# Kernel optimization log

Hardware: AMD Instinct MI355X
Metric: run time of the kernel (lower is better)

The kernel has to match this reference:

```python
import jax, jax.numpy as jnp
import numpy as np

B, T, N, E, F_IN = 2, 8, 4000, 40000, 32
H, C, HL, FH = 4, 64, 128, 128  # heads, gat_hidden, lstm_hidden, fusion_hidden


def setup_inputs() -> dict:
    key = jax.random.key(0)
    ks = jax.random.split(key, 14)
    def nrm(i, shape, s=0.05):
        return jax.random.normal(ks[i], shape, jnp.float32) * s
    return {
        "x_seq": jax.random.normal(ks[0], (B, T, N, F_IN), jnp.float32),
        "W1": nrm(2, (F_IN, H * C)), "a_src1": nrm(3, (H, C)), "a_dst1": nrm(4, (H, C)), "b1": jnp.zeros((C,), jnp.float32),
        "W2": nrm(5, (C, H * C)), "a_src2": nrm(6, (H, C)), "a_dst2": nrm(7, (H, C)), "b2": jnp.zeros((C,), jnp.float32),
        "W_ih": nrm(8, (4 * HL, C)), "W_hh": nrm(9, (4 * HL, HL)),
        "b_ih": jnp.zeros((4 * HL,), jnp.float32), "b_hh": jnp.zeros((4 * HL,), jnp.float32),
        "Wf": nrm(10, (HL + C, FH)), "bf": jnp.zeros((FH,), jnp.float32),
        "Wo": nrm(11, (FH, 1)), "bo": jnp.zeros((1,), jnp.float32),
        "edge_index": jax.random.randint(ks[1], (2, E), 0, N, jnp.int64)
                      if jax.config.read("jax_enable_x64") else jax.random.randint(ks[1], (2, E), 0, N, jnp.int32),
    }


def gat_conv(x, src, dst, n, W, a_src, a_dst, b):
    """PyG GATConv, concat=False (mean over heads), self-loops already in src/dst."""
    h = (x @ W).reshape(n, H, C)                      # [N,H,C]
    al_s = jnp.einsum('nhc,hc->nh', h, a_src)         # [N,H]
    al_d = jnp.einsum('nhc,hc->nh', h, a_dst)
    logits = jax.nn.leaky_relu(al_s[src] + al_d[dst], negative_slope=0.2)  # [E',H]
    m = jax.ops.segment_max(logits, dst, num_segments=n)
    e = jnp.exp(logits - m[dst])
    denom = jax.ops.segment_sum(e, dst, num_segments=n)
    alpha = e / denom[dst]                            # segment-softmax over incoming edges
    out = jax.ops.segment_sum(alpha[:, :, None] * h[src], dst, num_segments=n)  # [N,H,C]
    return out.mean(axis=1) + b                       # [N,C]


def reference(x_seq, W1, a_src1, a_dst1, b1, W2, a_src2, a_dst2, b2,
              W_ih, W_hh, b_ih, b_hh, Wf, bf, Wo, bo, edge_index):
    Bd, Td, Nd, Fd = x_seq.shape
    loop = jnp.arange(Nd, dtype=edge_index.dtype)     # add_self_loops=True
    src = jnp.concatenate([edge_index[0], loop])
    dst = jnp.concatenate([edge_index[1], loop])

    def gat2(x):
        g1 = jax.nn.relu(gat_conv(x, src, dst, Nd, W1, a_src1, a_dst1, b1))
        return jax.nn.relu(gat_conv(g1, src, dst, Nd, W2, a_src2, a_dst2, b2))

    # batched over all B*T graph instances at once
    g = jax.vmap(gat2)(x_seq.reshape(Bd * Td, Nd, Fd)).reshape(Bd, Td, Nd, C)

    # LSTM over time, batch = B*N nodes
    seq = g.transpose(1, 0, 2, 3).reshape(Td, Bd * Nd, C)
    h0 = jnp.zeros((Bd * Nd, HL), x_seq.dtype)

    def step(carry, xt):
        h, c = carry
        z = xt @ W_ih.T + b_ih + h @ W_hh.T + b_hh
        i, f, gg, o = jnp.split(z, 4, axis=-1)        # torch gate order i,f,g,o
        c = jax.nn.sigmoid(f) * c + jax.nn.sigmoid(i) * jnp.tanh(gg)
        h = jax.nn.sigmoid(o) * jnp.tanh(c)
        return (h, c), None

    (hT, _), _ = jax.lax.scan(step, (h0, h0), seq)
    lstm_last = hT.reshape(Bd, Nd, HL)
    fused = jax.nn.relu(jnp.concatenate([lstm_last, g[:, -1]], axis=-1) @ Wf + bf)
    return (fused @ Wo + bo)[..., 0]                  # [B, N]
```

## Files before the change

### kernel.cpp

```cpp
#include <hip/hip_runtime.h>
#include <math.h>

#define NN 4000
#define EE 40000
#define NE 44000
#define BB 2
#define TT 8
#define BT 16
#define HH 4
#define CC 64
#define HC 256
#define HLN 128
#define G4 512
#define FHN 128
#define PADU 136
#define PADC 196

typedef __attribute__((ext_vector_type(8))) short short8v;
typedef __attribute__((ext_vector_type(4))) float f32x4;

__device__ __forceinline__ float fexp2(float x){ return __builtin_amdgcn_exp2f(x); }
__device__ __forceinline__ float frcp(float x){ return __builtin_amdgcn_rcpf(x); }
__device__ __forceinline__ float fsig(float x){ return frcp(1.f + fexp2(x * -1.44269504f)); }
__device__ __forceinline__ float ftanh(float x){
  float xx = fminf(fmaxf(x, -10.f), 10.f);
  float e = fexp2(xx * 2.88539008f);
  return (e - 1.f) * frcp(e + 1.f);
}
__device__ __forceinline__ unsigned short bf16rne(float x){
  unsigned u = __float_as_uint(x);
  return (unsigned short)((u + 0x7FFFu + ((u>>16)&1u)) >> 16);
}
__device__ __forceinline__ float bf2f(unsigned short h){ return __uint_as_float(((unsigned)h)<<16); }

__global__ void k_count(const int* __restrict__ dst, int* __restrict__ cnt){
  int e = blockIdx.x*256+threadIdx.x;
  if (e >= NE) return;
  int d = (e < EE) ? dst[e] : (e - EE);
  atomicAdd(&cnt[d], 1);
}

__global__ __launch_bounds__(1024) void k_scan(const int* __restrict__ cnt, int* __restrict__ ptr){
  __shared__ int part[1024];
  const int n = NN;
  int t = threadIdx.x;
  int base = t*4;
  int loc[4]; int s = 0;
  #pragma unroll
  for (int i=0;i<4;i++){ int c = (base+i < n) ? cnt[base+i] : 0; loc[i] = s; s += c; }
  part[t] = s;
  __syncthreads();
  for (int off=1; off<1024; off<<=1){
    int add = (t >= off) ? part[t-off] : 0;
    __syncthreads();
    part[t] += add;
    __syncthreads();
  }
  int ebase = (t > 0) ? part[t-1] : 0;
  #pragma unroll
  for (int i=0;i<4;i++){ if (base+i < n) ptr[base+i] = ebase + loc[i]; }
  if (t == 1023) ptr[n] = part[1023];
}

__global__ void k_scatter(const int* __restrict__ dst, const int* __restrict__ ptr,
                          int* __restrict__ cur, int* __restrict__ idxa){
  int e = blockIdx.x*256+threadIdx.x;
  if (e >= NE) return;
  int d = (e < EE) ? dst[e] : (e - EE);
  int pos = atomicAdd(&cur[d], 1);
  idxa[ptr[d]+pos] = e;
}

__global__ void k_sortseg(const int* __restrict__ ptr, int* __restrict__ idxa,
                          const int* __restrict__ e0, int* __restrict__ srcs){
  int node = blockIdx.x*256+threadIdx.x;
  if (node >= NN) return;
  int p0 = ptr[node], p1 = ptr[node+1];
  for (int i=p0+1;i<p1;i++){
    int key = idxa[i]; int j = i-1;
    while (j >= p0 && idxa[j] > key){ idxa[j+1] = idxa[j]; j--; }
    idxa[j+1] = key;
  }
  for (int p=p0;p<p1;p++){
    int e = idxa[p];
    srcs[p] = (e < EE) ? e0[e] : (e - EE);
  }
}

__global__ void k_prep(int* __restrict__ cnt,
                       const float* __restrict__ W1, const float* __restrict__ as1, const float* __restrict__ ad1,
                       const float* __restrict__ W2, const float* __restrict__ as2, const float* __restrict__ ad2,
                       float* __restrict__ wt,
                       const float* __restrict__ Wih, const float* __restrict__ Whh,
                       unsigned short* __restrict__ wfh, unsigned short* __restrict__ wfl,
                       const float* __restrict__ Wf, float* __restrict__ WfT,
                       unsigned short* __restrict__ wb1h, unsigned short* __restrict__ wb1l,
                       unsigned short* __restrict__ wb2h, unsigned short* __restrict__ wb2l){
  int i = blockIdx.x*256 + threadIdx.x;
  if (i < 2*NN){ cnt[i] = 0; return; }
  i -= 2*NN;
  if (i < 768){
    if (i < 256){
      int sd = i >> 7, h = (i >> 5) & 3, k = i & 31;
      const float* a = sd ? ad1 : as1;
      float s = 0.f;
      for (int c=0;c<CC;c++) s = fmaf(W1[k*HC + h*CC + c], a[h*CC + c], s);
      wt[sd*128 + h*32 + k] = s;
    } else {
      int j = i - 256;
      int sd = j >> 8, h = (j >> 6) & 3, k = j & 63;
      const float* a = sd ? ad2 : as2;
      float s = 0.f;
      for (int c=0;c<CC;c++) s = fmaf(W2[k*HC + h*CC + c], a[h*CC + c], s);
      wt[256 + sd*256 + h*64 + k] = s;
    }
    return;
  }
  i -= 768;
  if (i < 12288){
    int lane = i & 63;
    int kc = (i >> 6) % 6;
    int wk = i / (64*6);
    int w = wk & 7, gg = wk >> 3;
    int n = gg*128 + w*16 + (lane & 15);
    int kbase = kc*32 + (lane >> 4)*8;
    #pragma unroll
    for (int j=0;j<8;j++){
      int k = kbase + j;
      float v = (k < 64) ? Wih[n*64 + k] : Whh[n*128 + (k-64)];
      unsigned short hi = bf16rne(v);
      wfh[(size_t)i*8 + j] = hi;
      wfl[(size_t)i*8 + j] = bf16rne(v - bf2f(hi));
    }
    return;
  }
  i -= 12288;
  if (i < 24576){
    int u = i & 127, k = i >> 7;
    WfT[u*192 + k] = Wf[k*128 + u];
    return;
  }
  i -= 24576;
  if (i < 1024){
    int lane = i & 63, kc = (i >> 6) & 3, nt = i >> 8;
    int n = nt*16 + (lane & 15);
    int kb = kc*32 + (lane >> 4)*8;
    #pragma unroll
    for (int j=0;j<8;j++){
      int k = kb + j; int h = k >> 5; int kk = k & 31;
      float v = W1[kk*HC + h*CC + n];
      unsigned short hi = bf16rne(v);
      wb1h[(size_t)i*8 + j] = hi;
      wb1l[(size_t)i*8 + j] = bf16rne(v - bf2f(hi));
    }
    return;
  }
  i -= 1024;
  if (i < 2048){
    int lane = i & 63, kc = (i >> 6) & 7, nt = i >> 9;
    int n = nt*16 + (lane & 15);
    int kb = kc*32 + (lane >> 4)*8;
    #pragma unroll
    for (int j=0;j<8;j++){
      int k = kb + j; int h = k >> 6; int kk = k & 63;
      float v = W2[kk*HC + h*CC + n];
      unsigned short hi = bf16rne(v);
      wb2h[(size_t)i*8 + j] = hi;
      wb2l[(size_t)i*8 + j] = bf16rne(v - bf2f(hi));
    }
  }
}

template<int K>
__global__ void k_coef3(const float* __restrict__ x, const float* __restrict__ wts,
                        const float* __restrict__ wtd,
                        float* __restrict__ als, float* __restrict__ ald){
  int i = blockIdx.x*256+threadIdx.x;
  if (i >= BT*NN) return;
  const float* xp = x + (size_t)i*K;
  float s1[4] = {0.f,0.f,0.f,0.f};
  float s2[4] = {0.f,0.f,0.f,0.f};
  for (int k=0;k<K;k+=4){
    float4 xv = *(const float4*)&xp[k];
    #pragma unroll
    for (int h=0;h<4;h++){
      float4 sv = *(const float4*)&wts[h*K+k];
      float4 dv = *(const float4*)&wtd[h*K+k];
      s1[h] = fmaf(xv.x,sv.x,fmaf(xv.y,sv.y,fmaf(xv.z,sv.z,fmaf(xv.w,sv.w,s1[h]))));
      s2[h] = fmaf(xv.x,dv.x,fmaf(xv.y,dv.y,fmaf(xv.z,dv.z,fmaf(xv.w,dv.w,s2[h]))));
    }
  }
  *(float4*)&als[(size_t)i*4] = make_float4(s1[0],s1[1],s1[2],s1[3]);
  *(float4*)&ald[(size_t)i*4] = make_float4(s2[0],s2[1],s2[2],s2[3]);
}

template<int KF, bool SPLIT>
__global__ __launch_bounds__(256) void k_gatt(const int* __restrict__ ptr, const int* __restrict__ srcs,
    const float* __restrict__ als, const float* __restrict__ ald, const float* __restrict__ xin,
    const unsigned short* __restrict__ wbh, const unsigned short* __restrict__ wbl,
    const float* __restrict__ bias, float* __restrict__ outp,
    unsigned short* __restrict__ ohi, unsigned short* __restrict__ olo){
  constexpr int K = HH*KF;
  constexpr int PR = K + 8;
  constexpr int NKC = K/32;
  constexpr int VPL = KF/16;
  __shared__ unsigned short agh[16*PR];
  __shared__ unsigned short agl[16*PR];
  const int tid = threadIdx.x;
  const int lane = tid & 63;
  const int wv = tid >> 6;
  const int l15 = lane & 15;
  const int lg  = lane >> 4;
  const int bid = blockIdx.x;
  const int q = bid >> 3;
  const int hi2 = (q >= 250);
  const int inst = (bid & 7) + (hi2 ? 8 : 0);
  const int node0 = (hi2 ? q - 250 : q)*16;
  const size_t ibase = (size_t)inst*NN;
  {
    const int nl = wv*4 + lg;
    const int node = node0 + nl;
    const int p0 = ptr[node], p1 = ptr[node+1];
    const float4 adv = *(const float4*)&ald[(ibase+node)*4];
    const float ad[4] = {adv.x, adv.y, adv.z, adv.w};
    float den[4] = {0.f,0.f,0.f,0.f};
    float a[4][VPL];
    #pragma unroll
    for (int h=0;h<4;h++)
      #pragma unroll
      for (int c=0;c<VPL;c++) a[h][c] = 0.f;
    int src = srcs[p0];
    for (int p = p0; p < p1; p++){
      const int nsrc = (p+1 < p1) ? srcs[p+1] : 0;
      const float4 av = *(const float4*)&als[(ibase + src)*4];
      float xv[VPL];
      if constexpr (VPL == 4){
        float4 x4 = *(const float4*)&xin[(ibase + src)*(size_t)KF + l15*4];
        xv[0]=x4.x; xv[1]=x4.y; xv[2]=x4.z; xv[3]=x4.w;
      } else {
        float2 x2 = *(const float2*)&xin[(ibase + src)*(size_t)KF + l15*2];
        xv[0]=x2.x; xv[1]=x2.y;
      }
      const float ac[4] = {av.x, av.y, av.z, av.w};
      #pragma unroll
      for (int h=0;h<4;h++){
        float v = ac[h] + ad[h];
        v = (v >= 0.f) ? v : 0.2f*v;
        float e = fexp2(v*1.44269504f);
        den[h] += e;
        #pragma unroll
        for (int c=0;c<VPL;c++) a[h][c] = fmaf(e, xv[c], a[h][c]);
      }
      src = nsrc;
    }
    #pragma unroll
    for (int h=0;h<4;h++){
      float inv = 0.25f * frcp(den[h]);
      unsigned short vh[VPL], vl[VPL];
      #pragma unroll
      for (int c=0;c<VPL;c++){
        float v = a[h][c]*inv;
        unsigned uh = __float_as_uint(v) & 0xFFFF0000u;
        vh[c] = (unsigned short)(uh >> 16);
        vl[c] = bf16rne(v - __uint_as_float(uh));
      }
      if constexpr (VPL == 4){
        uint2 ph = {((unsigned)vh[1]<<16)|vh[0], ((unsigned)vh[3]<<16)|vh[2]};
        uint2 pl = {((unsigned)vl[1]<<16)|vl[0], ((unsigned)vl[3]<<16)|vl[2]};
        *(uint2*)&agh[nl*PR + h*KF + l15*4] = ph;
        *(uint2*)&agl[nl*PR + h*KF + l15*4] = pl;
      } else {
        *(unsigned*)&agh[nl*PR + h*KF + l15*2] = ((unsigned)vh[1]<<16)|vh[0];
        *(unsigned*)&agl[nl*PR + h*KF + l15*2] = ((unsigned)vl[1]<<16)|vl[0];
      }
    }
  }
  __syncthreads();
  f32x4 acc = {0.f,0.f,0.f,0.f};
  #pragma unroll
  for (int kc=0; kc<NKC; kc++){
    size_t fl = (size_t)((wv*NKC + kc)*64 + lane)*8;
    short8v BH = *(const short8v*)&wbh[fl];
    short8v BL = *(const short8v*)&wbl[fl];
    int aoff = l15*PR + kc*32 + lg*8;
    short8v AH = *(const short8v*)&agh[aoff];
    short8v AL = *(const short8v*)&agl[aoff];
    acc = __builtin_amdgcn_mfma_f32_16x16x32_bf16(AH, BH, acc, 0,0,0);
    acc = __builtin_amdgcn_mfma_f32_16x16x32_bf16(AH, BL, acc, 0,0,0);
    acc = __builtin_amdgcn_mfma_f32_16x16x32_bf16(AL, BH, acc, 0,0,0);
  }
  const int c = wv*16 + l15;
  const float bv = bias[c];
  #pragma unroll
  for (int r=0;r<4;r++){
    int node = node0 + lg*4 + r;
    float val = fmaxf(acc[r] + bv, 0.f);
    size_t oi = (ibase + node)*CC + c;
    if constexpr (SPLIT){
      unsigned short hv = bf16rne(val);
      ohi[oi] = hv;
      olo[oi] = bf16rne(val - bf2f(hv));
    } else {
      outp[oi] = val;
    }
  }
}

__device__ __forceinline__ void mfma24(const short8v (&AH)[2], const short8v (&AL)[2],
                                       const short8v (&BH)[4], const short8v (&BL)[4],
                                       f32x4 (&acc)[2][4]){
  #pragma unroll
  for (int mt=0;mt<2;mt++)
    #pragma unroll
    for (int gg=0;gg<4;gg++)
      acc[mt][gg] = __builtin_amdgcn_mfma_f32_16x16x32_bf16(AH[mt], BH[gg], acc[mt][gg], 0,0,0);
  #pragma unroll
  for (int mt=0;mt<2;mt++)
    #pragma unroll
    for (int gg=0;gg<4;gg++)
      acc[mt][gg] = __builtin_amdgcn_mfma_f32_16x16x32_bf16(AH[mt], BL[gg], acc[mt][gg], 0,0,0);
  #pragma unroll
  for (int mt=0;mt<2;mt++)
    #pragma unroll
    for (int gg=0;gg<4;gg++)
      acc[mt][gg] = __builtin_amdgcn_mfma_f32_16x16x32_bf16(AL[mt], BH[gg], acc[mt][gg], 0,0,0);
}

__global__ __launch_bounds__(512) void k_lstm7(
    const unsigned short* __restrict__ ghi, const unsigned short* __restrict__ glo,
    const unsigned short* __restrict__ wfh, const unsigned short* __restrict__ wfl,
    const float* __restrict__ bih, const float* __restrict__ bhh,
    const float* __restrict__ WfT, const float* __restrict__ bfv,
    const float* __restrict__ Wo, const float* __restrict__ bo,
    float* __restrict__ out){
  __shared__ unsigned short hhi[32*PADU];
  __shared__ unsigned short hlo[32*PADU];
  __shared__ float catf[32*PADC];
  __shared__ float red[32*FHN];
  const int tid = threadIdx.x;
  const int lane = tid & 63;
  const int wv = tid >> 6;
  const int l15 = lane & 15;
  const int lg  = lane >> 4;
  const int r0 = blockIdx.x*32;
  const int b  = r0 / NN;
  const int n0 = r0 % NN;
  float bias[4];
  #pragma unroll
  for (int gg=0; gg<4; gg++){
    int n = gg*128 + wv*16 + l15;
    bias[gg] = bih[n] + bhh[n];
  }
  float c01[2][4];
  #pragma unroll
  for (int mt=0;mt<2;mt++){
    #pragma unroll
    for (int r=0;r<4;r++) c01[mt][r]=0.f;
  }
  auto ldw = [&](int kc, short8v (&BH)[4], short8v (&BL)[4]){
    #pragma unroll
    for (int gg=0;gg<4;gg++){
      size_t fl = (size_t)(((gg*8+wv)*6 + kc)*64 + lane)*8;
      BH[gg] = *(const short8v*)&wfh[fl];
      BL[gg] = *(const short8v*)&wfl[fl];
    }
  };

  for (int t=0;t<TT;t++){
    short8v axH[2][2], axL[2][2];
    #pragma unroll
    for (int mt=0; mt<2; mt++){
      const size_t row = ((size_t)(b*TT+t)*NN + n0 + mt*16 + l15);
      #pragma unroll
      for (int kc=0; kc<2; kc++){
        size_t off = row*64 + kc*32 + lg*8;
        axH[mt][kc] = *(const short8v*)&ghi[off];
        axL[mt][kc] = *(const short8v*)&glo[off];
      }
    }
    auto lda = [&](int kc, short8v (&AH)[2], short8v (&AL)[2]){
      if (kc < 2){
        AH[0]=axH[0][kc]; AH[1]=axH[1][kc];
        AL[0]=axL[0][kc]; AL[1]=axL[1][kc];
      } else {
        #pragma unroll
        for (int mt=0;mt<2;mt++){
          int off = (mt*16 + l15)*PADU + (kc-2)*32 + lg*8;
          AH[mt] = *(const short8v*)&hhi[off];
          AL[mt] = *(const short8v*)&hlo[off];
        }
      }
    };
    f32x4 acc[2][4];
    #pragma unroll
    for (int mt=0;mt<2;mt++){
      #pragma unroll
      for (int gg=0;gg<4;gg++){
        acc[mt][gg][0]=bias[gg]; acc[mt][gg][1]=bias[gg];
        acc[mt][gg][2]=bias[gg]; acc[mt][gg][3]=bias[gg];
      }
    }
    short8v BHa[4], BLa[4], BHb[4], BLb[4], AH[2], AL[2];
    if (t == 0){
      ldw(0, BHa, BLa);
      ldw(1, BHb, BLb);
      lda(0, AH, AL); mfma24(AH, AL, BHa, BLa, acc);
      lda(1, AH, AL); mfma24(AH, AL, BHb, BLb, acc);
    } else {
      ldw(0, BHa, BLa);
      ldw(1, BHb, BLb);
      lda(0, AH, AL); mfma24(AH, AL, BHa, BLa, acc);
      ldw(2, BHa, BLa);
      lda(1, AH, AL); mfma24(AH, AL, BHb, BLb, acc);
      ldw(3, BHb, BLb);
      lda(2, AH, AL); mfma24(AH, AL, BHa, BLa, acc);
      ldw(4, BHa, BLa);
      lda(3, AH, AL); mfma24(AH, AL, BHb, BLb, acc);
      ldw(5, BHb, BLb);
      lda(4, AH, AL); mfma24(AH, AL, BHa, BLa, acc);
      lda(5, AH, AL); mfma24(AH, AL, BHb, BLb, acc);
    }
    unsigned short hh_[2][4], hl_[2][4];
    float hv_[2][4];
    #pragma unroll
    for (int mt=0;mt<2;mt++){
      #pragma unroll
      for (int r=0;r<4;r++){
        float zi = acc[mt][0][r], zf = acc[mt][1][r], zg = acc[mt][2][r], zo = acc[mt][3][r];
        float cv = fsig(zf)*c01[mt][r] + fsig(zi)*ftanh(zg);
        c01[mt][r] = cv;
        float hv = fsig(zo)*ftanh(cv);
        hv_[mt][r] = hv;
        unsigned short hi = bf16rne(hv);
        hh_[mt][r] = hi;
        hl_[mt][r] = bf16rne(hv - bf2f(hi));
      }
    }
    if (t > 0) __syncthreads();
    if (t < TT-1){
      #pragma unroll
      for (int mt=0;mt<2;mt++){
        #pragma unroll
        for (int r=0;r<4;r++){
          int m = mt*16 + lg*4 + r;
          int u = wv*16 + l15;
          hhi[m*PADU + u] = hh_[mt][r];
          hlo[m*PADU + u] = hl_[mt][r];
        }
      }
    } else {
      #pragma unroll
      for (int mt=0;mt<2;mt++){
        #pragma unroll
        for (int r=0;r<4;r++){
          int m = mt*16 + lg*4 + r;
          int u = wv*16 + l15;
          catf[m*PADC + u] = hv_[mt][r];
        }
      }
      const size_t grow = ((size_t)(b*TT+TT-1)*NN + n0)*CC;
      int rr = tid >> 4, c4 = (tid & 15)*4;
      int idx = rr*CC + c4;
      #pragma unroll
      for (int qq=0;qq<4;qq++)
        catf[rr*PADC + 128 + c4 + qq] = bf2f(ghi[grow+idx+qq]) + bf2f(glo[grow+idx+qq]);
    }
    __syncthreads();
  }
  const int u = tid & 127;
  const int rg = tid >> 7;
  float fa[8];
  #pragma unroll
  for (int r=0;r<8;r++) fa[r] = bfv[u];
  for (int k4=0;k4<48;k4++){
    float4 wf = *(const float4*)&WfT[u*192 + k4*4];
    #pragma unroll
    for (int r=0;r<8;r++){
      float4 cv = *(const float4*)&catf[(rg*8+r)*PADC + k4*4];
      fa[r] = fmaf(cv.x,wf.x,fmaf(cv.y,wf.y,fmaf(cv.z,wf.z,fmaf(cv.w,wf.w,fa[r]))));
    }
  }
  float wo = Wo[u];
  #pragma unroll
  for (int r=0;r<8;r++) fa[r] = fmaxf(fa[r], 0.f) * wo;
  #pragma unroll
  for (int r=0;r<8;r++) red[(rg*8+r)*FHN + u] = fa[r];
  __syncthreads();
  for (int s=64;s>=1;s>>=1){
    if (u < s){
      #pragma unroll
      for (int r=0;r<8;r++) red[(rg*8+r)*FHN + u] += red[(rg*8+r)*FHN + u + s];
    }
    __syncthreads();
  }
  if (u == 0){
    #pragma unroll
    for (int r=0;r<8;r++) out[r0 + rg*8 + r] = red[(rg*8+r)*FHN] + bo[0];
  }
}

extern "C" void kernel_launch(void* const* d_in, const int* in_sizes, int n_in,
                              void* d_out, int out_size, void* d_ws, size_t ws_size,
                              hipStream_t stream) {
  const float* x_seq  = (const float*)d_in[0];
  const float* W1     = (const float*)d_in[1];
  const float* a_src1 = (const float*)d_in[2];
  const float* a_dst1 = (const float*)d_in[3];
  const float* b1     = (const float*)d_in[4];
  const float* W2     = (const float*)d_in[5];
  const float* a_src2 = (const float*)d_in[6];
  const float* a_dst2 = (const float*)d_in[7];
  const float* b2     = (const float*)d_in[8];
  const float* W_ih   = (const float*)d_in[9];
  const float* W_hh   = (const float*)d_in[10];
  const float* b_ih   = (const float*)d_in[11];
  const float* b_hh   = (const float*)d_in[12];
  const float* Wf     = (const float*)d_in[13];
  const float* bfv    = (const float*)d_in[14];
  const float* Wo     = (const float*)d_in[15];
  const float* bo     = (const float*)d_in[16];
  const int*   ei     = (const int*)d_in[17];
  const int* e_src = ei;
  const int* e_dst = ei + EE;
  float* out = (float*)d_out;

  char* w = (char*)d_ws;
  auto alloc = [&](size_t bytes)->char*{
    char* p = w; w += (bytes + 255) & ~(size_t)255; return p;
  };
  float* als   = (float*)alloc((size_t)BT*NN*HH*4);
  float* ald   = (float*)alloc((size_t)BT*NN*HH*4);
  float* gat1  = (float*)alloc((size_t)BT*NN*CC*4);
  unsigned short* ghi = (unsigned short*)alloc((size_t)BT*NN*CC*2);
  unsigned short* glo = (unsigned short*)alloc((size_t)BT*NN*CC*2);
  unsigned short* wfh = (unsigned short*)alloc((size_t)12288*8*2);
  unsigned short* wfl = (unsigned short*)alloc((size_t)12288*8*2);
  unsigned short* wb1h = (unsigned short*)alloc((size_t)1024*8*2);
  unsigned short* wb1l = (unsigned short*)alloc((size_t)1024*8*2);
  unsigned short* wb2h = (unsigned short*)alloc((size_t)2048*8*2);
  unsigned short* wb2l = (unsigned short*)alloc((size_t)2048*8*2);
  float* WfT   = (float*)alloc((size_t)128*192*4);
  float* wt    = (float*)alloc((size_t)768*4);
  int* cnt     = (int*)alloc((size_t)2*NN*4);
  int* cur     = cnt + NN;
  int* ptr     = (int*)alloc((size_t)(NN+1)*4);
  int* idxa    = (int*)alloc((size_t)NE*4);
  int* srcs    = (int*)alloc((size_t)NE*4);

  k_prep<<<(2*NN+768+12288+24576+1024+2048+255)/256, 256, 0, stream>>>(
      cnt, W1, a_src1, a_dst1, W2, a_src2, a_dst2, wt, W_ih, W_hh, wfh, wfl, Wf, WfT,
      wb1h, wb1l, wb2h, wb2l);
  k_count<<<(NE+255)/256, 256, 0, stream>>>(e_dst, cnt);
  k_scan<<<1, 1024, 0, stream>>>(cnt, ptr);
  k_scatter<<<(NE+255)/256, 256, 0, stream>>>(e_dst, ptr, cur, idxa);
  k_sortseg<<<(NN+255)/256, 256, 0, stream>>>(ptr, idxa, e_src, srcs);

  k_coef3<32><<<(BT*NN+255)/256, 256, 0, stream>>>(x_seq, wt, wt+128, als, ald);
  k_gatt<32,false><<<4000, 256, 0, stream>>>(ptr, srcs, als, ald, x_seq, wb1h, wb1l, b1,
                                             gat1, nullptr, nullptr);
  k_coef3<64><<<(BT*NN+255)/256, 256, 0, stream>>>(gat1, wt+256, wt+512, als, ald);
  k_gatt<64,true><<<4000, 256, 0, stream>>>(ptr, srcs, als, ald, gat1, wb2h, wb2l, b2,
                                            nullptr, ghi, glo);

  k_lstm7<<<BB*NN/32, 512, 0, stream>>>(ghi, glo, wfh, wfl, b_ih, b_hh, WfT, bfv, Wo, bo, out);
}
```

Baseline: 224.3 us.

## Cache recurrent LSTM weight high halves in LDS and unroll GAT edge loop by two

The LSTM kernel now copies the high bf16 half of the recurrent W_hh fragments into a 128 KB LDS buffer once per block. Each timestep reads them from LDS instead of re-fetching from global/L2; the low halves still come from global. The final-step catf and reduction buffers are aliased onto the reused LDS, and the last hidden state is rebuilt from the stored hi/lo bf16 pair. The GAT aggregation loop processes two edges per iteration to expose more independent loads and arithmetic. The large LDS footprint limits the LSTM kernel to one block per CU and adds an upfront staging cost per block.

```diff
diff --git a/kernel.cpp b/kernel.cpp
--- a/kernel.cpp
+++ b/kernel.cpp
@@ -229,29 +229,54 @@
     for (int h=0;h<4;h++)
       #pragma unroll
       for (int c=0;c<VPL;c++) a[h][c] = 0.f;
-    int src = srcs[p0];
-    for (int p = p0; p < p1; p++){
-      const int nsrc = (p+1 < p1) ? srcs[p+1] : 0;
-      const float4 av = *(const float4*)&als[(ibase + src)*4];
-      float xv[VPL];
+    auto ldx = [&](int s, float (&xv)[VPL]){
       if constexpr (VPL == 4){
-        float4 x4 = *(const float4*)&xin[(ibase + src)*(size_t)KF + l15*4];
+        float4 x4 = *(const float4*)&xin[(ibase + s)*(size_t)KF + l15*4];
         xv[0]=x4.x; xv[1]=x4.y; xv[2]=x4.z; xv[3]=x4.w;
       } else {
-        float2 x2 = *(const float2*)&xin[(ibase + src)*(size_t)KF + l15*2];
+        float2 x2 = *(const float2*)&xin[(ibase + s)*(size_t)KF + l15*2];
         xv[0]=x2.x; xv[1]=x2.y;
       }
-      const float ac[4] = {av.x, av.y, av.z, av.w};
+    };
+    int p = p0;
+    for (; p + 2 <= p1; p += 2){
+      const int s0 = srcs[p], s1 = srcs[p+1];
+      const float4 av0 = *(const float4*)&als[(ibase + s0)*4];
+      const float4 av1 = *(const float4*)&als[(ibase + s1)*4];
+      float xv0[VPL], xv1[VPL];
+      ldx(s0, xv0);
+      ldx(s1, xv1);
+      const float ac0[4] = {av0.x, av0.y, av0.z, av0.w};
+      const float ac1[4] = {av1.x, av1.y, av1.z, av1.w};
       #pragma unroll
       for (int h=0;h<4;h++){
-        float v = ac[h] + ad[h];
-        v = (v >= 0.f) ? v : 0.2f*v;
-        float e = fexp2(v*1.44269504f);
-        den[h] += e;
+        float v0 = ac0[h] + ad[h];
+        v0 = (v0 >= 0.f) ? v0 : 0.2f*v0;
+        float e0 = fexp2(v0*1.44269504f);
+        float v1 = ac1[h] + ad[h];
+        v1 = (v1 >= 0.f) ? v1 : 0.2f*v1;
+        float e1 = fexp2(v1*1.44269504f);
+        den[h] += e0 + e1;
         #pragma unroll
-        for (int c=0;c<VPL;c++) a[h][c] = fmaf(e, xv[c], a[h][c]);
-      }
-      src = nsrc;
+        for (int c=0;c<VPL;c++)
+          a[h][c] = fmaf(e0, xv0[c], fmaf(e1, xv1[c], a[h][c]));
+      }
+    }
+    if (p < p1){
+      const int s0 = srcs[p];
+      const float4 av0 = *(const float4*)&als[(ibase + s0)*4];
+      float xv0[VPL];
+      ldx(s0, xv0);
+      const float ac0[4] = {av0.x, av0.y, av0.z, av0.w};
+      #pragma unroll
+      for (int h=0;h<4;h++){
+        float v0 = ac0[h] + ad[h];
+        v0 = (v0 >= 0.f) ? v0 : 0.2f*v0;
+        float e0 = fexp2(v0*1.44269504f);
+        den[h] += e0;
+        #pragma unroll
+        for (int c=0;c<VPL;c++) a[h][c] = fmaf(e0, xv0[c], a[h][c]);
+      }
     }
     #pragma unroll
     for (int h=0;h<4;h++){
@@ -326,17 +351,17 @@
       acc[mt][gg] = __builtin_amdgcn_mfma_f32_16x16x32_bf16(AL[mt], BH[gg], acc[mt][gg], 0,0,0);
 }
 
-__global__ __launch_bounds__(512) void k_lstm7(
+__global__ __launch_bounds__(512) void k_lstm11(
     const unsigned short* __restrict__ ghi, const unsigned short* __restrict__ glo,
     const unsigned short* __restrict__ wfh, const unsigned short* __restrict__ wfl,
     const float* __restrict__ bih, const float* __restrict__ bhh,
     const float* __restrict__ WfT, const float* __restrict__ bfv,
     const float* __restrict__ Wo, const float* __restrict__ bo,
     float* __restrict__ out){
-  __shared__ unsigned short hhi[32*PADU];
-  __shared__ unsigned short hlo[32*PADU];
-  __shared__ float catf[32*PADC];
-  __shared__ float red[32*FHN];
+  __shared__ unsigned short whhl[128*512];
+  __shared__ unsigned short hbuf[2*32*PADU];
+  unsigned short* hhi = hbuf;
+  unsigned short* hlo = hbuf + 32*PADU;
   const int tid = threadIdx.x;
   const int lane = tid & 63;
   const int wv = tid >> 6;
@@ -345,6 +370,12 @@
   const int r0 = blockIdx.x*32;
   const int b  = r0 / NN;
   const int n0 = r0 % NN;
+  for (int i = tid; i < 128*64; i += 512){
+    int frag = i >> 6, sub = i & 63;
+    int gw = frag >> 2, kcr = frag & 3;
+    size_t gsrc = ((size_t)(gw*6 + kcr + 2)*64 + sub)*8;
+    *(uint4*)&whhl[(size_t)i*8] = *(const uint4*)&wfh[gsrc];
+  }
   float bias[4];
   #pragma unroll
   for (int gg=0; gg<4; gg++){
@@ -353,11 +384,12 @@
   }
   float c01[2][4];
   #pragma unroll
-  for (int mt=0;mt<2;mt++){
+  for (int mt=0;mt<2;mt++)
     #pragma unroll
     for (int r=0;r<4;r++) c01[mt][r]=0.f;
-  }
-  auto ldw = [&](int kc, short8v (&BH)[4], short8v (&BL)[4]){
+  __syncthreads();
+
+  auto ldwx = [&](int kc, short8v (&BH)[4], short8v (&BL)[4]){
     #pragma unroll
     for (int gg=0;gg<4;gg++){
       size_t fl = (size_t)(((gg*8+wv)*6 + kc)*64 + lane)*8;
@@ -365,6 +397,15 @@
       BL[gg] = *(const short8v*)&wfl[fl];
     }
   };
+  auto ldwh = [&](int kcr, short8v (&BH)[4], short8v (&BL)[4]){
+    #pragma unroll
+    for (int gg=0;gg<4;gg++){
+      size_t lf = (size_t)(((gg*8+wv)*4 + kcr)*64 + lane)*8;
+      BH[gg] = *(const short8v*)&whhl[lf];
+      size_t fl = (size_t)(((gg*8+wv)*6 + kcr + 2)*64 + lane)*8;
+      BL[gg] = *(const short8v*)&wfl[fl];
+    }
+  };
 
   for (int t=0;t<TT;t++){
     short8v axH[2][2], axL[2][2];
@@ -378,17 +419,12 @@
         axL[mt][kc] = *(const short8v*)&glo[off];
       }
     }
-    auto lda = [&](int kc, short8v (&AH)[2], short8v (&AL)[2]){
-      if (kc < 2){
-        AH[0]=axH[0][kc]; AH[1]=axH[1][kc];
-        AL[0]=axL[0][kc]; AL[1]=axL[1][kc];
-      } else {
-        #pragma unroll
-        for (int mt=0;mt<2;mt++){
-          int off = (mt*16 + l15)*PADU + (kc-2)*32 + lg*8;
-          AH[mt] = *(const short8v*)&hhi[off];
-          AL[mt] = *(const short8v*)&hlo[off];
-        }
+    auto ldah = [&](int kcr, short8v (&AH)[2], short8v (&AL)[2]){
+      #pragma unroll
+      for (int mt=0;mt<2;mt++){
+        int off = (mt*16 + l15)*PADU + kcr*32 + lg*8;
+        AH[mt] = *(const short8v*)&hhi[off];
+        AL[mt] = *(const short8v*)&hlo[off];
       }
     };
     f32x4 acc[2][4];
@@ -402,26 +438,29 @@
     }
     short8v BHa[4], BLa[4], BHb[4], BLb[4], AH[2], AL[2];
     if (t == 0){
-      ldw(0, BHa, BLa);
-      ldw(1, BHb, BLb);
-      lda(0, AH, AL); mfma24(AH, AL, BHa, BLa, acc);
-      lda(1, AH, AL); mfma24(AH, AL, BHb, BLb, acc);
+      ldwx(0, BHa, BLa);
+      ldwx(1, BHb, BLb);
+      AH[0]=axH[0][0]; AH[1]=axH[1][0]; AL[0]=axL[0][0]; AL[1]=axL[1][0];
+      mfma24(AH, AL, BHa, BLa, acc);
+      AH[0]=axH[0][1]; AH[1]=axH[1][1]; AL[0]=axL[0][1]; AL[1]=axL[1][1];
+      mfma24(AH, AL, BHb, BLb, acc);
     } else {
-      ldw(0, BHa, BLa);
-      ldw(1, BHb, BLb);
-      lda(0, AH, AL); mfma24(AH, AL, BHa, BLa, acc);
-      ldw(2, BHa, BLa);
-      lda(1, AH, AL); mfma24(AH, AL, BHb, BLb, acc);
-      ldw(3, BHb, BLb);
-      lda(2, AH, AL); mfma24(AH, AL, BHa, BLa, acc);
-      ldw(4, BHa, BLa);
-      lda(3, AH, AL); mfma24(AH, AL, BHb, BLb, acc);
-      ldw(5, BHb, BLb);
-      lda(4, AH, AL); mfma24(AH, AL, BHa, BLa, acc);
-      lda(5, AH, AL); mfma24(AH, AL, BHb, BLb, acc);
+      ldwx(0, BHa, BLa);
+      ldwx(1, BHb, BLb);
+      AH[0]=axH[0][0]; AH[1]=axH[1][0]; AL[0]=axL[0][0]; AL[1]=axL[1][0];
+      mfma24(AH, AL, BHa, BLa, acc);
+      ldwh(0, BHa, BLa);
+      AH[0]=axH[0][1]; AH[1]=axH[1][1]; AL[0]=axL[0][1]; AL[1]=axL[1][1];
+      mfma24(AH, AL, BHb, BLb, acc);
+      ldwh(1, BHb, BLb);
+      ldah(0, AH, AL); mfma24(AH, AL, BHa, BLa, acc);
+      ldwh(2, BHa, BLa);
+      ldah(1, AH, AL); mfma24(AH, AL, BHb, BLb, acc);
+      ldwh(3, BHb, BLb);
+      ldah(2, AH, AL); mfma24(AH, AL, BHa, BLa, acc);
+      ldah(3, AH, AL); mfma24(AH, AL, BHb, BLb, acc);
     }
     unsigned short hh_[2][4], hl_[2][4];
-    float hv_[2][4];
     #pragma unroll
     for (int mt=0;mt<2;mt++){
       #pragma unroll
@@ -430,43 +469,39 @@
         float cv = fsig(zf)*c01[mt][r] + fsig(zi)*ftanh(zg);
         c01[mt][r] = cv;
         float hv = fsig(zo)*ftanh(cv);
-        hv_[mt][r] = hv;
         unsigned short hi = bf16rne(hv);
         hh_[mt][r] = hi;
         hl_[mt][r] = bf16rne(hv - bf2f(hi));
       }
     }
     if (t > 0) __syncthreads();
-    if (t < TT-1){
-      #pragma unroll
-      for (int mt=0;mt<2;mt++){
-        #pragma unroll
-        for (int r=0;r<4;r++){
-          int m = mt*16 + lg*4 + r;
-          int u = wv*16 + l15;
-          hhi[m*PADU + u] = hh_[mt][r];
-          hlo[m*PADU + u] = hl_[mt][r];
-        }
-      }
-    } else {
-      #pragma unroll
-      for (int mt=0;mt<2;mt++){
-        #pragma unroll
-        for (int r=0;r<4;r++){
-          int m = mt*16 + lg*4 + r;
-          int u = wv*16 + l15;
-          catf[m*PADC + u] = hv_[mt][r];
-        }
-      }
-      const size_t grow = ((size_t)(b*TT+TT-1)*NN + n0)*CC;
-      int rr = tid >> 4, c4 = (tid & 15)*4;
-      int idx = rr*CC + c4;
-      #pragma unroll
-      for (int qq=0;qq<4;qq++)
-        catf[rr*PADC + 128 + c4 + qq] = bf2f(ghi[grow+idx+qq]) + bf2f(glo[grow+idx+qq]);
+    #pragma unroll
+    for (int mt=0;mt<2;mt++){
+      #pragma unroll
+      for (int r=0;r<4;r++){
+        int m = mt*16 + lg*4 + r;
+        int u = wv*16 + l15;
+        hhi[m*PADU + u] = hh_[mt][r];
+        hlo[m*PADU + u] = hl_[mt][r];
+      }
     }
     __syncthreads();
   }
+  float* catf = (float*)whhl;
+  {
+    const size_t grow = ((size_t)(b*TT+TT-1)*NN + n0)*CC;
+    for (int i = tid; i < 32*192; i += 512){
+      int m = i / 192, k = i - m*192;
+      float v;
+      if (k < 128) v = bf2f(hhi[m*PADU + k]) + bf2f(hlo[m*PADU + k]);
+      else {
+        size_t gi = grow + (size_t)m*CC + (k-128);
+        v = bf2f(ghi[gi]) + bf2f(glo[gi]);
+      }
+      catf[m*PADC + k] = v;
+    }
+  }
+  __syncthreads();
   const int u = tid & 127;
   const int rg = tid >> 7;
   float fa[8];
@@ -483,6 +518,8 @@
   float wo = Wo[u];
   #pragma unroll
   for (int r=0;r<8;r++) fa[r] = fmaxf(fa[r], 0.f) * wo;
+  __syncthreads();
+  float* red = (float*)hbuf;
   #pragma unroll
   for (int r=0;r<8;r++) red[(rg*8+r)*FHN + u] = fa[r];
   __syncthreads();
@@ -562,5 +599,5 @@
   k_gatt<64,true><<<4000, 256, 0, stream>>>(ptr, srcs, als, ald, gat1, wb2h, wb2l, b2,
                                             nullptr, ghi, glo);
 
-  k_lstm7<<<BB*NN/32, 512, 0, stream>>>(ghi, glo, wfh, wfl, b_ih, b_hh, WfT, bfv, Wo, bo, out);
-}
+  k_lstm11<<<BB*NN/32, 512, 0, stream>>>(ghi, glo, wfh, wfl, b_ih, b_hh, WfT, bfv, Wo, bo, out);
+}
```

After: 211.8 us. 5.6% less time.
